# Kernel tuning notes

Hardware: AMD Instinct MI355X
Metric: run time of the kernel (lower is better)

Reference implementation:

```python
import jax, jax.numpy as jnp
import numpy as np
import math

B, S, IN_DIM, EMBED, HEADS, WINDOW = 2, 2048, 512, 512, 8, 64
HEAD_DIM = EMBED // HEADS
NEG = -9e15


def setup_inputs() -> dict:
    key = jax.random.key(0)
    k1, k2, k3, k4 = jax.random.split(key, 4)
    x = jax.random.normal(k1, (B, S, IN_DIM), dtype=jnp.float32)
    padding_mask = jax.random.randint(k2, (B, S), 0, 2, dtype=jnp.int32)
    # xavier-uniform-style init for projections (torch Linear convention transposed)
    lim_qkv = math.sqrt(6.0 / (IN_DIM + 3 * EMBED))
    Wqkv = jax.random.uniform(k3, (IN_DIM, 3 * EMBED), minval=-lim_qkv, maxval=lim_qkv, dtype=jnp.float32)
    bqkv = jnp.zeros((3 * EMBED,), dtype=jnp.float32)
    lim_o = math.sqrt(6.0 / (EMBED + EMBED))
    Wo = jax.random.uniform(k4, (EMBED, EMBED), minval=-lim_o, maxval=lim_o, dtype=jnp.float32)
    bo = jnp.zeros((EMBED,), dtype=jnp.float32)
    return {"x": x, "padding_mask": padding_mask, "Wqkv": Wqkv, "bqkv": bqkv, "Wo": Wo, "bo": bo}


def reference(x, padding_mask, Wqkv, bqkv, Wo, bo):
    b, s, _ = x.shape
    half = WINDOW // 2
    w1 = WINDOW + 1  # band width per query

    qkv = x @ Wqkv + bqkv                               # [B,S,3E]
    qkv = qkv.reshape(b, s, HEADS, 3, HEAD_DIM)
    q = jnp.transpose(qkv[..., 0, :], (0, 2, 1, 3))     # [B,H,S,Dh]
    k = jnp.transpose(qkv[..., 1, :], (0, 2, 1, 3))
    v = jnp.transpose(qkv[..., 2, :], (0, 2, 1, 3))

    # banded key indices: query i attends keys in [i-half, i+half]
    offs = jnp.arange(-half, half + 1)                  # [W1]
    idx = jnp.arange(s)[:, None] + offs[None, :]        # [S,W1]
    valid = (idx >= 0) & (idx < s)
    idxc = jnp.clip(idx, 0, s - 1)

    k_band = k[:, :, idxc, :]                           # [B,H,S,W1,Dh]
    v_band = v[:, :, idxc, :]
    scores = jnp.einsum('bhsd,bhswd->bhsw', q, k_band) / math.sqrt(HEAD_DIM)

    pm = padding_mask != 0                              # [B,S]
    band_mask = valid[None, :, :] & pm[:, idxc]         # [B,S,W1]
    scores = jnp.where(band_mask[:, None, :, :], scores, NEG)
    attn = jax.nn.softmax(scores, axis=-1)              # [B,H,S,W1]

    out = jnp.einsum('bhsw,bhswd->bhsd', attn, v_band)  # [B,H,S,Dh]
    out = out * pm[:, None, :, None].astype(out.dtype)  # zero padded queries

    out = jnp.transpose(out, (0, 2, 1, 3)).reshape(b, s, EMBED)
    return out @ Wo + bo
```

## Files before the change

kernel.cpp:

```cpp
#include <hip/hip_runtime.h>
#include <hip/hip_bf16.h>

typedef __bf16 bf16;
typedef __bf16 bf16x4 __attribute__((ext_vector_type(4)));
typedef __bf16 bf16x8 __attribute__((ext_vector_type(8)));
typedef float f32x4 __attribute__((ext_vector_type(4)));

#define NEGV -9.0e15f

#define GLD16(gp, lp)                                                    \
  __builtin_amdgcn_global_load_lds(                                     \
      (const __attribute__((address_space(1))) void*)(gp),              \
      (__attribute__((address_space(3))) void*)(lp), 16, 0, 0)


__global__ __launch_bounds__(256) void k_prep(
    const float* __restrict__ x, const float* __restrict__ Wqkv, const float* __restrict__ Wo,
    bf16* __restrict__ xb, bf16* __restrict__ WqkvT, bf16* __restrict__ WoT) {
  const int bid = blockIdx.x, tid = threadIdx.x;
  if (bid < 2048) {
    int i = bid * 1024 + tid * 4;
    float4 v = *(const float4*)(x + i);
    bf16x4 o;
    o[0] = (bf16)v.x; o[1] = (bf16)v.y; o[2] = (bf16)v.z; o[3] = (bf16)v.w;
    *(bf16x4*)(xb + i) = o;
    return;
  }
  __shared__ float tl[32][33];
  const float* src; bf16* dst; int N, t; bool remap;
  if (bid < 2816) { t = bid - 2048; src = Wqkv; dst = WqkvT; N = 1536; remap = true; }
  else            { t = bid - 2816; src = Wo;   dst = WoT;   N = 512;  remap = false; }
  const int tk = t & 15, tn = t >> 4;
  const int c = tid & 31, r0 = tid >> 5;
  for (int rr = 0; rr < 4; ++rr) {
    int row = r0 + rr * 8;
    tl[row][c] = src[(size_t)(tk * 32 + row) * N + tn * 32 + c];
  }
  __syncthreads();
  for (int rr = 0; rr < 4; ++rr) {
    int row = r0 + rr * 8;
    int nn = tn * 32 + row;
    int np = nn;
    if (remap) {
      int h = nn / 192, r2 = nn - h * 192, sel = r2 >> 6, d = r2 & 63;
      np = sel * 512 + h * 64 + d;
    }
    dst[(size_t)np * 512 + tk * 32 + c] = (bf16)tl[c][row];
  }
}


__global__ __launch_bounds__(128) void k_gemm_qkv(
    const bf16* __restrict__ A, const bf16* __restrict__ BT, const float* __restrict__ bias,
    bf16* __restrict__ Qb, bf16* __restrict__ Kb, bf16* __restrict__ VTb) {
  __shared__ __align__(16) char As[16384];
  __shared__ __align__(16) char Bs[8192];
  const int m0 = blockIdx.x * 128, n0 = blockIdx.y * 64;
  const int sel = blockIdx.y >> 3;
  const bool isV = (sel == 2);
  const int tid = threadIdx.x, wave = tid >> 6, lane = tid & 63;
  const int lr = lane & 15, lg = lane >> 4;
  const int wr = wave * 64;
  const int srow = lane >> 3;
  const int srcsw = ((lane & 7) ^ (srow & 7)) << 4;
  const int kxor = (lr & 7) << 4;
  const char* Ab = (const char*)A;
  const char* Bb = (const char*)BT;
  f32x4 acc[4][4] = {};

  for (int kt = 0; kt < 512; kt += 64) {
    __syncthreads();
#pragma unroll
    for (int t = 0; t < 8; ++t) {
      int chunk = wave * 8 + t;
      GLD16(Ab + (size_t)(m0 + chunk * 8 + srow) * 1024 + kt * 2 + srcsw,
            As + chunk * 1024);
    }
#pragma unroll
    for (int t = 0; t < 4; ++t) {
      int chunk = wave * 4 + t;
      GLD16(Bb + (size_t)(n0 + chunk * 8 + srow) * 1024 + kt * 2 + srcsw,
            Bs + chunk * 1024);
    }
    __syncthreads();
#pragma unroll
    for (int kk = 0; kk < 2; ++kk) {
      bf16x8 af[4], bfr[4];
      int colb = kk * 64 + lg * 16;
#pragma unroll
      for (int m = 0; m < 4; ++m)
        af[m] = *(const bf16x8*)(As + (wr + m * 16 + lr) * 128 + (colb ^ kxor));
#pragma unroll
      for (int n = 0; n < 4; ++n)
        bfr[n] = *(const bf16x8*)(Bs + (n * 16 + lr) * 128 + (colb ^ kxor));
      if (!isV) {
#pragma unroll
        for (int m = 0; m < 4; ++m)
#pragma unroll
          for (int n = 0; n < 4; ++n)
            acc[m][n] = __builtin_amdgcn_mfma_f32_16x16x32_bf16(af[m], bfr[n], acc[m][n], 0, 0, 0);
      } else {
#pragma unroll
        for (int m = 0; m < 4; ++m)
#pragma unroll
          for (int n = 0; n < 4; ++n)
            acc[m][n] = __builtin_amdgcn_mfma_f32_16x16x32_bf16(bfr[n], af[m], acc[m][n], 0, 0, 0);
      }
    }
  }

  if (!isV) {
    bf16* Dst = sel ? Kb : Qb;
    float bv[4]; int hh[4], dd[4];
#pragma unroll
    for (int n = 0; n < 4; ++n) {
      int gn = n0 + n * 16 + lr;
      hh[n] = (gn >> 6) & 7; dd[n] = gn & 63;
      bv[n] = bias[hh[n] * 192 + sel * 64 + dd[n]];
    }
#pragma unroll
    for (int m = 0; m < 4; ++m)
#pragma unroll
      for (int r = 0; r < 4; ++r) {
        int gm = m0 + wr + m * 16 + lg * 4 + r;
        int b = gm >> 11, s = gm & 2047;
#pragma unroll
        for (int n = 0; n < 4; ++n) {
          float v = acc[m][n][r] + bv[n];
          Dst[((size_t)(b * 8 + hh[n]) * 2048 + s) * 64 + dd[n]] = (bf16)v;
        }
      }
  } else {
#pragma unroll
    for (int m = 0; m < 4; ++m) {
      int gm = m0 + wr + m * 16 + lr;
      int b = gm >> 11, s = gm & 2047;
#pragma unroll
      for (int n = 0; n < 4; ++n)
#pragma unroll
        for (int r = 0; r < 4; ++r) {
          int gn = n0 + n * 16 + lg * 4 + r;
          int h = (gn >> 6) & 7, d = gn & 63;
          float v = acc[m][n][r] + bias[h * 192 + 128 + d];
          VTb[((size_t)(b * 8 + h) * 64 + d) * 2048 + s] = (bf16)v;
        }
    }
  }
}


__global__ __launch_bounds__(256) void k_attn(
    const bf16* __restrict__ Qb, const bf16* __restrict__ Kb, const bf16* __restrict__ VTb,
    const int* __restrict__ pmask, bf16* __restrict__ AO) {
  __shared__ __align__(16) char Qs[64 * 128];
  __shared__ __align__(16) char Ks[128 * 128];
  __shared__ __align__(16) char VTs[64 * 256];
  __shared__ __align__(16) char Ps[64 * 256];
  __shared__ float pmk[128];

  const int qb = blockIdx.x, bh = blockIdx.y;
  const int b = bh >> 3, h = bh & 7;
  const int q0 = qb * 64, kstart = q0 - 32;
  const int tid = threadIdx.x, wave = tid >> 6, lane = tid & 63;
  const int lr = lane & 15, lg = lane >> 4;

  const bf16* Qg = Qb + (size_t)bh * (2048 * 64);
  const bf16* Kg = Kb + (size_t)bh * (2048 * 64);
  const bf16* Vg = VTb + (size_t)bh * (64 * 2048);

  const int srow8 = lane >> 3;
  const int srcsw8 = ((lane & 7) ^ (srow8 & 7)) << 4;
#pragma unroll
  for (int t = 0; t < 2; ++t) {
    int chunk = wave * 2 + t;
    int row = q0 + chunk * 8 + srow8;
    GLD16((const char*)Qg + (size_t)row * 128 + srcsw8, Qs + chunk * 1024);
  }
#pragma unroll
  for (int t = 0; t < 4; ++t) {
    int chunk = wave * 4 + t;
    int row = chunk * 8 + srow8;
    int sk = kstart + row;
    sk = sk < 0 ? 0 : (sk > 2047 ? 2047 : sk);
    GLD16((const char*)Kg + (size_t)sk * 128 + srcsw8, Ks + chunk * 1024);
  }
  {
    int srow4 = lane >> 4, cb = (lane & 15) << 4;
#pragma unroll
    for (int t = 0; t < 4; ++t) {
      int chunk = wave * 4 + t;
      int d = chunk * 4 + srow4;
      int csw = cb ^ ((d & 7) << 4);
      int sl = kstart + (csw >> 1);
      sl = sl < 0 ? 0 : (sl > 2040 ? 2040 : sl);
      GLD16((const char*)Vg + (size_t)d * 4096 + (size_t)sl * 2, VTs + chunk * 1024);
    }
  }
  if (tid < 128) {
    int sk = kstart + tid;
    pmk[tid] = (sk >= 0 && sk < 2048 && pmask[b * 2048 + sk] != 0) ? 0.0f : NEGV;
  }
  __syncthreads();

  const int kxor = (lr & 7) << 4;
  f32x4 sc[8] = {};
#pragma unroll
  for (int kk = 0; kk < 2; ++kk) {
    int colb = kk * 64 + lg * 16;
    int qrow = wave * 16 + lr;
    bf16x8 qf = *(const bf16x8*)(Qs + qrow * 128 + (colb ^ kxor));
#pragma unroll
    for (int nt = 0; nt < 8; ++nt) {
      int krow = nt * 16 + lr;
      bf16x8 kf = *(const bf16x8*)(Ks + krow * 128 + (colb ^ kxor));
      sc[nt] = __builtin_amdgcn_mfma_f32_16x16x32_bf16(qf, kf, sc[nt], 0, 0, 0);
    }
  }

  float msk[8];
#pragma unroll
  for (int nt = 0; nt < 8; ++nt) msk[nt] = pmk[nt * 16 + lr];
  float rsum[4] = {0.f, 0.f, 0.f, 0.f};
#pragma unroll
  for (int nt = 0; nt < 8; ++nt) {
    int j = nt * 16 + lr;
#pragma unroll
    for (int r = 0; r < 4; ++r) {
      int qrow = wave * 16 + lg * 4 + r;
      float v = fmaf(sc[nt][r], 0.125f, msk[nt]);
      v = ((unsigned)(j - qrow) <= 64u) ? v : NEGV;
      float p = __expf(v);
      sc[nt][r] = p;
      rsum[r] += p;
    }
  }
#pragma unroll
  for (int off = 1; off < 16; off <<= 1)
#pragma unroll
    for (int r = 0; r < 4; ++r)
      rsum[r] += __shfl_xor(rsum[r], off);
#pragma unroll
  for (int r = 0; r < 4; ++r) rsum[r] = fmaxf(rsum[r], 1e-30f);

#pragma unroll
  for (int nt = 0; nt < 8; ++nt)
#pragma unroll
    for (int r = 0; r < 4; ++r) {
      int qrow = wave * 16 + lg * 4 + r;
      int colb = (nt * 16 + lr) * 2;
      *(bf16*)(Ps + qrow * 256 + (colb ^ ((qrow & 7) << 4))) = (bf16)sc[nt][r];
    }
  __syncthreads();

  f32x4 oacc[4] = {};
#pragma unroll
  for (int ks = 0; ks < 4; ++ks) {
    int colb = ks * 64 + lg * 16;
    int prow = wave * 16 + lr;
    bf16x8 pf = *(const bf16x8*)(Ps + prow * 256 + (colb ^ ((prow & 7) << 4)));
#pragma unroll
    for (int n = 0; n < 4; ++n) {
      int vrow = n * 16 + lr;
      bf16x8 vf = *(const bf16x8*)(VTs + vrow * 256 + (colb ^ ((vrow & 7) << 4)));
      oacc[n] = __builtin_amdgcn_mfma_f32_16x16x32_bf16(pf, vf, oacc[n], 0, 0, 0);
    }
  }

  float inv[4];
#pragma unroll
  for (int r = 0; r < 4; ++r) inv[r] = 1.0f / rsum[r];
#pragma unroll
  for (int r = 0; r < 4; ++r) {
    int qrow = wave * 16 + lg * 4 + r;
    float s2 = (pmk[32 + qrow] == 0.0f) ? inv[r] : 0.0f;
#pragma unroll
    for (int n = 0; n < 4; ++n)
      AO[(size_t)(b * 2048 + q0 + qrow) * 512 + h * 64 + n * 16 + lr] = (bf16)(oacc[n][r] * s2);
  }
}


__global__ __launch_bounds__(256) void k_gemm_out(
    const bf16* __restrict__ A, const bf16* __restrict__ BT, const float* __restrict__ bias,
    float* __restrict__ C) {
  __shared__ __align__(16) char As[16384];
  __shared__ __align__(16) char Bs[8192];
  const int m0 = blockIdx.x * 128, n0 = blockIdx.y * 64;
  const int tid = threadIdx.x, wave = tid >> 6, lane = tid & 63;
  const int wr = (wave >> 1) * 64, wc = (wave & 1) * 32;
  const int lr = lane & 15, lg = lane >> 4;
  const int srow = lane >> 3;
  const int srcsw = ((lane & 7) ^ (srow & 7)) << 4;
  const int kxor = (lr & 7) << 4;
  const char* Ab = (const char*)A;
  const char* Bb = (const char*)BT;
  f32x4 acc[4][2] = {};

  for (int kt = 0; kt < 512; kt += 64) {
    __syncthreads();
#pragma unroll
    for (int t = 0; t < 4; ++t) {
      int chunk = wave * 4 + t;
      GLD16(Ab + (size_t)(m0 + chunk * 8 + srow) * 1024 + kt * 2 + srcsw,
            As + chunk * 1024);
    }
#pragma unroll
    for (int t = 0; t < 2; ++t) {
      int chunk = wave * 2 + t;
      GLD16(Bb + (size_t)(n0 + chunk * 8 + srow) * 1024 + kt * 2 + srcsw,
            Bs + chunk * 1024);
    }
    __syncthreads();
#pragma unroll
    for (int kk = 0; kk < 2; ++kk) {
      bf16x8 af[4], bfr[2];
      int colb = kk * 64 + lg * 16;
#pragma unroll
      for (int m = 0; m < 4; ++m)
        af[m] = *(const bf16x8*)(As + (wr + m * 16 + lr) * 128 + (colb ^ kxor));
#pragma unroll
      for (int n = 0; n < 2; ++n)
        bfr[n] = *(const bf16x8*)(Bs + (wc + n * 16 + lr) * 128 + (colb ^ kxor));
#pragma unroll
      for (int m = 0; m < 4; ++m)
#pragma unroll
        for (int n = 0; n < 2; ++n)
          acc[m][n] = __builtin_amdgcn_mfma_f32_16x16x32_bf16(af[m], bfr[n], acc[m][n], 0, 0, 0);
    }
  }

  float bv0 = bias[n0 + wc + lr], bv1 = bias[n0 + wc + 16 + lr];
#pragma unroll
  for (int m = 0; m < 4; ++m)
#pragma unroll
    for (int n = 0; n < 2; ++n)
#pragma unroll
      for (int r = 0; r < 4; ++r) {
        int gm = m0 + wr + m * 16 + lg * 4 + r;
        int gn = n0 + wc + n * 16 + lr;
        C[(size_t)gm * 512 + gn] = acc[m][n][r] + (n ? bv1 : bv0);
      }
}


extern "C" void kernel_launch(void* const* d_in, const int* in_sizes, int n_in,
                              void* d_out, int out_size, void* d_ws, size_t ws_size,
                              hipStream_t stream) {
  const float* x     = (const float*)d_in[0];
  const int*   pmask = (const int*)d_in[1];
  const float* Wqkv  = (const float*)d_in[2];
  const float* bqkv  = (const float*)d_in[3];
  const float* Wo    = (const float*)d_in[4];
  const float* bo    = (const float*)d_in[5];
  float* out = (float*)d_out;

  char* ws = (char*)d_ws;
  bf16* xb    = (bf16*)(ws);
  bf16* WqkvT = (bf16*)(ws + 4194304);
  bf16* WoT   = (bf16*)(ws + 5767168);
  bf16* Qb    = (bf16*)(ws + 6291456);
  bf16* Kb    = (bf16*)(ws + 10485760);
  bf16* VTb   = (bf16*)(ws + 14680064);
  bf16* AO    = (bf16*)(ws + 18874368);

  k_prep<<<3072, 256, 0, stream>>>(x, Wqkv, Wo, xb, WqkvT, WoT);

  dim3 g1(32, 24);
  k_gemm_qkv<<<g1, 128, 0, stream>>>(xb, WqkvT, bqkv, Qb, Kb, VTb);

  dim3 ga(32, 16);
  k_attn<<<ga, 256, 0, stream>>>(Qb, Kb, VTb, pmask, AO);

  dim3 g2(32, 8);
  k_gemm_out<<<g2, 256, 0, stream>>>(AO, WoT, bo, out);
}
```

Before: 47.36 us.

## Double-buffer QKV GEMM, split-K output GEMM, load Q directly to registers

The QKV GEMM moves to 256 threads with a 2x2 wave tiling and double-buffered LDS staging, so the next K-tile's global-to-LDS loads overlap the current tile's MFMAs. The output GEMM uses 512 threads split into two K-halves, with partial sums reduced through LDS before the store. The attention kernel reads Q fragments straight from global memory into registers instead of staging them in LDS. The XOR swizzle on LDS tiles is removed in both GEMMs, which may bring back bank conflicts, and the larger LDS footprint may lower occupancy.

```diff
diff --git a/kernel.cpp b/kernel.cpp
--- a/kernel.cpp
+++ b/kernel.cpp
@@ -50,71 +50,81 @@
 }
 
 
-__global__ __launch_bounds__(128) void k_gemm_qkv(
+__global__ __launch_bounds__(256) void k_gemm_qkv(
     const bf16* __restrict__ A, const bf16* __restrict__ BT, const float* __restrict__ bias,
     bf16* __restrict__ Qb, bf16* __restrict__ Kb, bf16* __restrict__ VTb) {
-  __shared__ __align__(16) char As[16384];
-  __shared__ __align__(16) char Bs[8192];
+  __shared__ __align__(16) char lds[49152];
   const int m0 = blockIdx.x * 128, n0 = blockIdx.y * 64;
   const int sel = blockIdx.y >> 3;
   const bool isV = (sel == 2);
   const int tid = threadIdx.x, wave = tid >> 6, lane = tid & 63;
+  const int wr = (wave >> 1) * 64, wc = (wave & 1) * 32;
   const int lr = lane & 15, lg = lane >> 4;
-  const int wr = wave * 64;
-  const int srow = lane >> 3;
-  const int srcsw = ((lane & 7) ^ (srow & 7)) << 4;
-  const int kxor = (lr & 7) << 4;
+  const int srow = lane >> 3, scolb = (lane & 7) << 4;
   const char* Ab = (const char*)A;
   const char* Bb = (const char*)BT;
-  f32x4 acc[4][4] = {};
-
-  for (int kt = 0; kt < 512; kt += 64) {
-    __syncthreads();
-#pragma unroll
-    for (int t = 0; t < 8; ++t) {
-      int chunk = wave * 8 + t;
-      GLD16(Ab + (size_t)(m0 + chunk * 8 + srow) * 1024 + kt * 2 + srcsw,
-            As + chunk * 1024);
-    }
+  f32x4 acc[4][2] = {};
+
+  auto STAGE = [&](int buf, int kb) {
+    char* Asb = lds + buf * 16384;
+    char* Bsb = lds + 32768 + buf * 8192;
 #pragma unroll
     for (int t = 0; t < 4; ++t) {
       int chunk = wave * 4 + t;
-      GLD16(Bb + (size_t)(n0 + chunk * 8 + srow) * 1024 + kt * 2 + srcsw,
-            Bs + chunk * 1024);
-    }
-    __syncthreads();
+      GLD16(Ab + (size_t)(m0 + chunk * 8 + srow) * 1024 + kb + scolb, Asb + chunk * 1024);
+    }
+#pragma unroll
+    for (int t = 0; t < 2; ++t) {
+      int chunk = wave * 2 + t;
+      GLD16(Bb + (size_t)(n0 + chunk * 8 + srow) * 1024 + kb + scolb, Bsb + chunk * 1024);
+    }
+  };
+
+  STAGE(0, 0);
+  asm volatile("s_waitcnt vmcnt(0)" ::: "memory");
+  __syncthreads();
+
+  for (int it = 0; it < 8; ++it) {
+    const int cur = it & 1;
+    if (it < 7) STAGE(cur ^ 1, (it + 1) * 128);
+    const char* As = lds + cur * 16384;
+    const char* Bs = lds + 32768 + cur * 8192;
 #pragma unroll
     for (int kk = 0; kk < 2; ++kk) {
-      bf16x8 af[4], bfr[4];
-      int colb = kk * 64 + lg * 16;
+      bf16x8 af[4], bfr[2];
 #pragma unroll
       for (int m = 0; m < 4; ++m)
-        af[m] = *(const bf16x8*)(As + (wr + m * 16 + lr) * 128 + (colb ^ kxor));
-#pragma unroll
-      for (int n = 0; n < 4; ++n)
-        bfr[n] = *(const bf16x8*)(Bs + (n * 16 + lr) * 128 + (colb ^ kxor));
+        af[m] = *(const bf16x8*)(As + (wr + m * 16 + lr) * 128 + kk * 64 + lg * 16);
+#pragma unroll
+      for (int n = 0; n < 2; ++n)
+        bfr[n] = *(const bf16x8*)(Bs + (wc + n * 16 + lr) * 128 + kk * 64 + lg * 16);
       if (!isV) {
 #pragma unroll
         for (int m = 0; m < 4; ++m)
 #pragma unroll
-          for (int n = 0; n < 4; ++n)
+          for (int n = 0; n < 2; ++n)
             acc[m][n] = __builtin_amdgcn_mfma_f32_16x16x32_bf16(af[m], bfr[n], acc[m][n], 0, 0, 0);
       } else {
 #pragma unroll
         for (int m = 0; m < 4; ++m)
 #pragma unroll
-          for (int n = 0; n < 4; ++n)
+          for (int n = 0; n < 2; ++n)
             acc[m][n] = __builtin_amdgcn_mfma_f32_16x16x32_bf16(bfr[n], af[m], acc[m][n], 0, 0, 0);
       }
     }
+    if (it < 7) {
+      asm volatile("s_waitcnt vmcnt(0)" ::: "memory");
+      __builtin_amdgcn_s_barrier();
+      asm volatile("" ::: "memory");
+    }
   }
 
   if (!isV) {
     bf16* Dst = sel ? Kb : Qb;
-    float bv[4]; int hh[4], dd[4];
-#pragma unroll
-    for (int n = 0; n < 4; ++n) {
-      int gn = n0 + n * 16 + lr;
+    float bv[2]; int hh[2], dd[2];
+#pragma unroll
+    for (int n = 0; n < 2; ++n) {
+      int gn = n0 + wc + n * 16 + lr;
       hh[n] = (gn >> 6) & 7; dd[n] = gn & 63;
       bv[n] = bias[hh[n] * 192 + sel * 64 + dd[n]];
     }
@@ -125,7 +135,7 @@
         int gm = m0 + wr + m * 16 + lg * 4 + r;
         int b = gm >> 11, s = gm & 2047;
 #pragma unroll
-        for (int n = 0; n < 4; ++n) {
+        for (int n = 0; n < 2; ++n) {
           float v = acc[m][n][r] + bv[n];
           Dst[((size_t)(b * 8 + hh[n]) * 2048 + s) * 64 + dd[n]] = (bf16)v;
         }
@@ -136,10 +146,10 @@
       int gm = m0 + wr + m * 16 + lr;
       int b = gm >> 11, s = gm & 2047;
 #pragma unroll
-      for (int n = 0; n < 4; ++n)
+      for (int n = 0; n < 2; ++n)
 #pragma unroll
         for (int r = 0; r < 4; ++r) {
-          int gn = n0 + n * 16 + lg * 4 + r;
+          int gn = n0 + wc + n * 16 + lg * 4 + r;
           int h = (gn >> 6) & 7, d = gn & 63;
           float v = acc[m][n][r] + bias[h * 192 + 128 + d];
           VTb[((size_t)(b * 8 + h) * 64 + d) * 2048 + s] = (bf16)v;
@@ -152,7 +162,6 @@
 __global__ __launch_bounds__(256) void k_attn(
     const bf16* __restrict__ Qb, const bf16* __restrict__ Kb, const bf16* __restrict__ VTb,
     const int* __restrict__ pmask, bf16* __restrict__ AO) {
-  __shared__ __align__(16) char Qs[64 * 128];
   __shared__ __align__(16) char Ks[128 * 128];
   __shared__ __align__(16) char VTs[64 * 256];
   __shared__ __align__(16) char Ps[64 * 256];
@@ -170,12 +179,6 @@
 
   const int srow8 = lane >> 3;
   const int srcsw8 = ((lane & 7) ^ (srow8 & 7)) << 4;
-#pragma unroll
-  for (int t = 0; t < 2; ++t) {
-    int chunk = wave * 2 + t;
-    int row = q0 + chunk * 8 + srow8;
-    GLD16((const char*)Qg + (size_t)row * 128 + srcsw8, Qs + chunk * 1024);
-  }
 #pragma unroll
   for (int t = 0; t < 4; ++t) {
     int chunk = wave * 4 + t;
@@ -196,6 +199,10 @@
       GLD16((const char*)Vg + (size_t)d * 4096 + (size_t)sl * 2, VTs + chunk * 1024);
     }
   }
+  const size_t qoff = (size_t)(q0 + wave * 16 + lr) * 64;
+  bf16x8 qf0 = *(const bf16x8*)(Qg + qoff + lg * 8);
+  bf16x8 qf1 = *(const bf16x8*)(Qg + qoff + 32 + lg * 8);
+
   if (tid < 128) {
     int sk = kstart + tid;
     pmk[tid] = (sk >= 0 && sk < 2048 && pmask[b * 2048 + sk] != 0) ? 0.0f : NEGV;
@@ -206,9 +213,8 @@
   f32x4 sc[8] = {};
 #pragma unroll
   for (int kk = 0; kk < 2; ++kk) {
+    bf16x8 qf = kk ? qf1 : qf0;
     int colb = kk * 64 + lg * 16;
-    int qrow = wave * 16 + lr;
-    bf16x8 qf = *(const bf16x8*)(Qs + qrow * 128 + (colb ^ kxor));
 #pragma unroll
     for (int nt = 0; nt < 8; ++nt) {
       int krow = nt * 16 + lr;
@@ -280,47 +286,45 @@
 }
 
 
-__global__ __launch_bounds__(256) void k_gemm_out(
+__global__ __launch_bounds__(512) void k_gemm_out(
     const bf16* __restrict__ A, const bf16* __restrict__ BT, const float* __restrict__ bias,
     float* __restrict__ C) {
-  __shared__ __align__(16) char As[16384];
-  __shared__ __align__(16) char Bs[8192];
+  __shared__ __align__(16) char lds[49152];
   const int m0 = blockIdx.x * 128, n0 = blockIdx.y * 64;
   const int tid = threadIdx.x, wave = tid >> 6, lane = tid & 63;
-  const int wr = (wave >> 1) * 64, wc = (wave & 1) * 32;
+  const int kg = wave >> 2, w2 = wave & 3;
+  const int wr = (w2 >> 1) * 64, wc = (w2 & 1) * 32;
   const int lr = lane & 15, lg = lane >> 4;
-  const int srow = lane >> 3;
-  const int srcsw = ((lane & 7) ^ (srow & 7)) << 4;
-  const int kxor = (lr & 7) << 4;
+  const int srow = lane >> 3, scolb = (lane & 7) << 4;
   const char* Ab = (const char*)A;
   const char* Bb = (const char*)BT;
+  char* As = lds + kg * 16384;
+  char* Bs = lds + 32768 + kg * 8192;
   f32x4 acc[4][2] = {};
 
-  for (int kt = 0; kt < 512; kt += 64) {
+  for (int it = 0; it < 4; ++it) {
+    int kb = kg * 512 + it * 128;
     __syncthreads();
 #pragma unroll
     for (int t = 0; t < 4; ++t) {
-      int chunk = wave * 4 + t;
-      GLD16(Ab + (size_t)(m0 + chunk * 8 + srow) * 1024 + kt * 2 + srcsw,
-            As + chunk * 1024);
+      int chunk = w2 * 4 + t;
+      GLD16(Ab + (size_t)(m0 + chunk * 8 + srow) * 1024 + kb + scolb, As + chunk * 1024);
     }
 #pragma unroll
     for (int t = 0; t < 2; ++t) {
-      int chunk = wave * 2 + t;
-      GLD16(Bb + (size_t)(n0 + chunk * 8 + srow) * 1024 + kt * 2 + srcsw,
-            Bs + chunk * 1024);
+      int chunk = w2 * 2 + t;
+      GLD16(Bb + (size_t)(n0 + chunk * 8 + srow) * 1024 + kb + scolb, Bs + chunk * 1024);
     }
     __syncthreads();
 #pragma unroll
     for (int kk = 0; kk < 2; ++kk) {
       bf16x8 af[4], bfr[2];
-      int colb = kk * 64 + lg * 16;
 #pragma unroll
       for (int m = 0; m < 4; ++m)
-        af[m] = *(const bf16x8*)(As + (wr + m * 16 + lr) * 128 + (colb ^ kxor));
+        af[m] = *(const bf16x8*)(As + (wr + m * 16 + lr) * 128 + kk * 64 + lg * 16);
 #pragma unroll
       for (int n = 0; n < 2; ++n)
-        bfr[n] = *(const bf16x8*)(Bs + (wc + n * 16 + lr) * 128 + (colb ^ kxor));
+        bfr[n] = *(const bf16x8*)(Bs + (wc + n * 16 + lr) * 128 + kk * 64 + lg * 16);
 #pragma unroll
       for (int m = 0; m < 4; ++m)
 #pragma unroll
@@ -329,17 +333,30 @@
     }
   }
 
-  float bv0 = bias[n0 + wc + lr], bv1 = bias[n0 + wc + 16 + lr];
-#pragma unroll
-  for (int m = 0; m < 4; ++m)
-#pragma unroll
-    for (int n = 0; n < 2; ++n)
-#pragma unroll
-      for (int r = 0; r < 4; ++r) {
-        int gm = m0 + wr + m * 16 + lg * 4 + r;
-        int gn = n0 + wc + n * 16 + lr;
-        C[(size_t)gm * 512 + gn] = acc[m][n][r] + (n ? bv1 : bv0);
+  __syncthreads();
+  if (kg == 1) {
+#pragma unroll
+    for (int m = 0; m < 4; ++m)
+#pragma unroll
+      for (int n = 0; n < 2; ++n)
+        *(f32x4*)(lds + (((m * 2 + n) * 256 + w2 * 64 + lane) << 4)) = acc[m][n];
+  }
+  __syncthreads();
+  if (kg == 0) {
+    float bv0 = bias[n0 + wc + lr], bv1 = bias[n0 + wc + 16 + lr];
+#pragma unroll
+    for (int m = 0; m < 4; ++m)
+#pragma unroll
+      for (int n = 0; n < 2; ++n) {
+        acc[m][n] += *(const f32x4*)(lds + (((m * 2 + n) * 256 + w2 * 64 + lane) << 4));
+#pragma unroll
+        for (int r = 0; r < 4; ++r) {
+          int gm = m0 + wr + m * 16 + lg * 4 + r;
+          int gn = n0 + wc + n * 16 + lr;
+          C[(size_t)gm * 512 + gn] = acc[m][n][r] + (n ? bv1 : bv0);
+        }
       }
+  }
 }
 
 
@@ -366,11 +383,11 @@
   k_prep<<<3072, 256, 0, stream>>>(x, Wqkv, Wo, xb, WqkvT, WoT);
 
   dim3 g1(32, 24);
-  k_gemm_qkv<<<g1, 128, 0, stream>>>(xb, WqkvT, bqkv, Qb, Kb, VTb);
+  k_gemm_qkv<<<g1, 256, 0, stream>>>(xb, WqkvT, bqkv, Qb, Kb, VTb);
 
   dim3 ga(32, 16);
   k_attn<<<ga, 256, 0, stream>>>(Qb, Kb, VTb, pmask, AO);
 
   dim3 g2(32, 8);
-  k_gemm_out<<<g2, 256, 0, stream>>>(AO, WoT, bo, out);
-}
+  k_gemm_out<<<g2, 512, 0, stream>>>(AO, WoT, bo, out);
+}
```

Result: faster. 41.11 us (-13.2%).
